# Performance work log

Measured on AMD Instinct MI355X. Metric: run time of the kernel, lower is better.

## Reference

```python
import jax, jax.numpy as jnp
import numpy as np

B, S, H = 32, 1, 1024            # decode: one query token per sequence
NH, HD = 16, 64                  # num_heads, head_dim
BS = 16                          # cache block size
MAX_KV = 2048                    # max sequence length in cache
BLOCKS_PER_SEQ = MAX_KV // BS    # 128
NUM_BLOCKS = B * BLOCKS_PER_SEQ  # 4096 physical blocks
SCALE = HD ** -0.5


def setup_inputs() -> dict:
    key = jax.random.key(0)
    ks = jax.random.split(key, 8)
    hidden_states = jax.random.normal(ks[0], (B, S, H), jnp.float32) * 0.02
    # kv_cache[0] = key cache, kv_cache[1] = value cache; paged layout
    kv_cache = jax.random.normal(ks[1], (2, NUM_BLOCKS, BS, NH, HD), jnp.float32) * 0.02
    # each sequence owns a contiguous run of physical blocks (valid block table)
    block_tables = jnp.arange(NUM_BLOCKS, dtype=jnp.int32).reshape(B, BLOCKS_PER_SEQ)
    seq_lens = jax.random.randint(ks[2], (B,), 1, MAX_KV + 1, dtype=jnp.int32)
    w_attn = jax.random.normal(ks[3], (H, 3 * H), jnp.float32) * 0.02
    b_attn = jax.random.normal(ks[4], (3 * H,), jnp.float32) * 0.02
    w_proj = jax.random.normal(ks[5], (H, H), jnp.float32) * 0.02
    b_proj = jax.random.normal(ks[6], (H,), jnp.float32) * 0.02
    return {"hidden_states": hidden_states, "kv_cache": kv_cache,
            "block_tables": block_tables, "seq_lens": seq_lens,
            "w_attn": w_attn, "b_attn": b_attn,
            "w_proj": w_proj, "b_proj": b_proj}


def reference(hidden_states, kv_cache, block_tables, seq_lens,
              w_attn, b_attn, w_proj, b_proj):
    # qkv projection (c_attn); only q is consumed by the paged-attention decode
    qkv = hidden_states @ w_attn + b_attn                      # [B, S, 3H]
    q = qkv[..., :H].reshape(B, S, NH, HD)                     # [B, 1, NH, HD]

    # block-table gather of paged KV cache
    # kv_cache[0][block_tables]: [B, BLOCKS_PER_SEQ, BS, NH, HD]
    keys = kv_cache[0][block_tables].reshape(B, MAX_KV, NH, HD)
    vals = kv_cache[1][block_tables].reshape(B, MAX_KV, NH, HD)

    scores = jnp.einsum('bsnd,bknd->bnsk', q, keys) * SCALE    # [B, NH, S, MAX_KV]
    valid = jnp.arange(MAX_KV)[None, :] < seq_lens[:, None]    # [B, MAX_KV]
    scores = jnp.where(valid[:, None, None, :], scores, -jnp.inf)
    probs = jax.nn.softmax(scores, axis=-1)

    attn = jnp.einsum('bnsk,bknd->bsnd', probs, vals).reshape(B, S, H)
    return attn @ w_proj + b_proj                              # [B, S, H]
```

## Files before the change

### kernel.cpp

```cpp
#include <hip/hip_runtime.h>
#include <hip/hip_bf16.h>

#define BATCH 32
#define HID 1024
#define NH 16
#define HD 64
#define BS 16
#define MAX_KV 2048
#define BPS 128
#define NUM_BLOCKS 4096
#define SCALE 0.125f

#define SPLITS 8
#define CHUNK 256
#define KSPLIT 4
#define KCHUNK (HID / KSPLIT)

__global__ __launch_bounds__(256) void init_kernel(
    const float* __restrict__ b_attn, const float* __restrict__ b_proj,
    float* __restrict__ q, float* __restrict__ out)
{
    const int i = blockIdx.x * 256 + threadIdx.x;
    const int col = i & (HID - 1);
    q[i]   = b_attn[col];
    out[i] = b_proj[col];
}

__global__ __launch_bounds__(256) void gemv_kernel(
    const float* __restrict__ x,
    const float* __restrict__ w,
    float* __restrict__ y,
    int wstride)
{
    const int colg = blockIdx.x;
    const int kz = blockIdx.y;
    const int tid = threadIdx.x, wave = tid >> 6, lane = tid & 63;
    const int col = colg * 64 + lane;

    __shared__ float s_x[BATCH * KCHUNK];
    for (int i = tid; i < BATCH * KCHUNK; i += 256) {
        const int bb = i >> 8, kk = i & (KCHUNK - 1);
        s_x[bb * KCHUNK + kk] = x[bb * HID + kz * KCHUNK + kk];
    }
    __syncthreads();

    float acc[BATCH];
    #pragma unroll
    for (int b = 0; b < BATCH; ++b) acc[b] = 0.f;

    const int kw = wave * (KCHUNK / 4);
    const float* wp = w + (size_t)(kz * KCHUNK + kw) * wstride + col;
    #pragma unroll 4
    for (int j = 0; j < KCHUNK / 4; ++j) {
        const float wv = wp[(size_t)j * wstride];
        #pragma unroll
        for (int b = 0; b < BATCH; ++b)
            acc[b] += s_x[b * KCHUNK + kw + j] * wv;
    }

    __syncthreads();
    #pragma unroll
    for (int b = 0; b < BATCH; ++b)
        s_x[wave * 2048 + b * 64 + lane] = acc[b];
    __syncthreads();
    for (int i = tid; i < BATCH * 64; i += 256) {
        const int bb = i >> 6, cc = i & 63;
        const float v = s_x[0 * 2048 + bb * 64 + cc] + s_x[1 * 2048 + bb * 64 + cc]
                      + s_x[2 * 2048 + bb * 64 + cc] + s_x[3 * 2048 + bb * 64 + cc];
        atomicAdd(&y[bb * HID + colg * 64 + cc], v);
    }
}

__global__ __launch_bounds__(256) void attn_split_kernel(
    const float* __restrict__ q,
    const float* __restrict__ kv,
    const int* __restrict__ block_tables,
    const int* __restrict__ seq_lens,
    float* __restrict__ part)
{
    const int h = blockIdx.x, b = blockIdx.y, s = blockIdx.z;
    const int tid = threadIdx.x, wave = tid >> 6, lane = tid & 63;
    const int pos_sub = lane >> 4;
    const int d4 = lane & 15;

    float* my_part = part + ((size_t)(b * NH + h) * SPLITS + s) * (HD + 2);
    const int n = seq_lens[b];
    const int p0 = s * CHUNK;

    if (p0 >= n) {
        if (tid < HD) my_part[tid] = 0.f;
        if (tid == 0) { my_part[HD] = -1e30f; my_part[HD + 1] = 0.f; }
        return;
    }
    const int cnt = min(n - p0, CHUNK);

    __shared__ float s_sc[CHUNK];
    __shared__ int   s_bt[CHUNK / BS];
    __shared__ float s_redm[4], s_redl[4];
    __shared__ float s_part[4 * HD];

    if (tid < CHUNK / BS) s_bt[tid] = block_tables[b * BPS + p0 / BS + tid];
    const float4 qv = *reinterpret_cast<const float4*>(
        q + (size_t)(b * NH + h) * HD + d4 * 4);
    __syncthreads();

    const size_t v_off = (size_t)NUM_BLOCKS * BS * NH * HD;

    for (int base = wave * 8; base < cnt; base += 32) {
        const int pa = base + 2 * pos_sub;
        const int pb = pa + 1;
        float sa = 0.f, sb = 0.f;
        if (pa < cnt) {
            const float* kp = kv + (((size_t)s_bt[pa >> 4] * BS + (pa & 15)) * NH + h) * HD + d4 * 4;
            const float4 k4 = *reinterpret_cast<const float4*>(kp);
            sa = qv.x * k4.x + qv.y * k4.y + qv.z * k4.z + qv.w * k4.w;
        }
        if (pb < cnt) {
            const float* kp = kv + (((size_t)s_bt[pb >> 4] * BS + (pb & 15)) * NH + h) * HD + d4 * 4;
            const float4 k4 = *reinterpret_cast<const float4*>(kp);
            sb = qv.x * k4.x + qv.y * k4.y + qv.z * k4.z + qv.w * k4.w;
        }
        sa += __shfl_xor(sa, 1); sb += __shfl_xor(sb, 1);
        sa += __shfl_xor(sa, 2); sb += __shfl_xor(sb, 2);
        sa += __shfl_xor(sa, 4); sb += __shfl_xor(sb, 4);
        sa += __shfl_xor(sa, 8); sb += __shfl_xor(sb, 8);
        if (d4 == 0) {
            if (pa < cnt) s_sc[pa] = sa * SCALE;
            if (pb < cnt) s_sc[pb] = sb * SCALE;
        }
    }
    __syncthreads();

    const float v = (tid < cnt) ? s_sc[tid] : -1e30f;
    float m = v;
    #pragma unroll
    for (int msk = 32; msk; msk >>= 1) m = fmaxf(m, __shfl_xor(m, msk));
    if (lane == 0) s_redm[wave] = m;
    __syncthreads();
    m = fmaxf(fmaxf(s_redm[0], s_redm[1]), fmaxf(s_redm[2], s_redm[3]));

    const float e = (tid < cnt) ? __expf(v - m) : 0.f;
    if (tid < cnt) s_sc[tid] = e;
    float l = e;
    #pragma unroll
    for (int msk = 32; msk; msk >>= 1) l += __shfl_xor(l, msk);
    if (lane == 0) s_redl[wave] = l;
    __syncthreads();
    const float l_tot = s_redl[0] + s_redl[1] + s_redl[2] + s_redl[3];

    float4 acc = {0.f, 0.f, 0.f, 0.f};
    for (int base = wave * 8; base < cnt; base += 32) {
        const int pa = base + 2 * pos_sub;
        const int pb = pa + 1;
        if (pa < cnt) {
            const float* vp = kv + v_off + (((size_t)s_bt[pa >> 4] * BS + (pa & 15)) * NH + h) * HD + d4 * 4;
            const float4 v4 = *reinterpret_cast<const float4*>(vp);
            const float w = s_sc[pa];
            acc.x += w * v4.x; acc.y += w * v4.y; acc.z += w * v4.z; acc.w += w * v4.w;
        }
        if (pb < cnt) {
            const float* vp = kv + v_off + (((size_t)s_bt[pb >> 4] * BS + (pb & 15)) * NH + h) * HD + d4 * 4;
            const float4 v4 = *reinterpret_cast<const float4*>(vp);
            const float w = s_sc[pb];
            acc.x += w * v4.x; acc.y += w * v4.y; acc.z += w * v4.z; acc.w += w * v4.w;
        }
    }
    acc.x += __shfl_xor(acc.x, 16); acc.y += __shfl_xor(acc.y, 16);
    acc.z += __shfl_xor(acc.z, 16); acc.w += __shfl_xor(acc.w, 16);
    acc.x += __shfl_xor(acc.x, 32); acc.y += __shfl_xor(acc.y, 32);
    acc.z += __shfl_xor(acc.z, 32); acc.w += __shfl_xor(acc.w, 32);
    if (pos_sub == 0) {
        s_part[wave * HD + d4 * 4 + 0] = acc.x;
        s_part[wave * HD + d4 * 4 + 1] = acc.y;
        s_part[wave * HD + d4 * 4 + 2] = acc.z;
        s_part[wave * HD + d4 * 4 + 3] = acc.w;
    }
    __syncthreads();
    if (tid < HD) {
        my_part[tid] = s_part[tid] + s_part[HD + tid] +
                       s_part[2 * HD + tid] + s_part[3 * HD + tid];
    }
    if (tid == 0) { my_part[HD] = m; my_part[HD + 1] = l_tot; }
}

__global__ __launch_bounds__(64) void attn_reduce_kernel(
    const float* __restrict__ part,
    float* __restrict__ attn_out)
{
    const int h = blockIdx.x, b = blockIdx.y, d = threadIdx.x;
    const float* pp = part + (size_t)(b * NH + h) * SPLITS * (HD + 2);
    float m = -1e30f;
    #pragma unroll
    for (int s = 0; s < SPLITS; ++s) m = fmaxf(m, pp[s * (HD + 2) + HD]);
    float o = 0.f, l = 0.f;
    #pragma unroll
    for (int s = 0; s < SPLITS; ++s) {
        const float a = __expf(pp[s * (HD + 2) + HD] - m);
        o += a * pp[s * (HD + 2) + d];
        l += a * pp[s * (HD + 2) + HD + 1];
    }
    attn_out[(size_t)b * HID + h * HD + d] = o / l;
}

extern "C" void kernel_launch(void* const* d_in, const int* in_sizes, int n_in,
                              void* d_out, int out_size, void* d_ws, size_t ws_size,
                              hipStream_t stream) {
    const float* hs     = (const float*)d_in[0];
    const float* kv     = (const float*)d_in[1];
    const int*   bt     = (const int*)d_in[2];
    const int*   sl     = (const int*)d_in[3];
    const float* w_attn = (const float*)d_in[4];
    const float* b_attn = (const float*)d_in[5];
    const float* w_proj = (const float*)d_in[6];
    const float* b_proj = (const float*)d_in[7];
    float* out = (float*)d_out;

    float* q    = (float*)d_ws;
    float* attn = q + BATCH * HID;
    float* part = attn + BATCH * HID;

    init_kernel<<<BATCH * HID / 256, 256, 0, stream>>>(b_attn, b_proj, q, out);
    gemv_kernel<<<dim3(HID / 64, KSPLIT), 256, 0, stream>>>(hs, w_attn, q, 3 * HID);
    attn_split_kernel<<<dim3(NH, BATCH, SPLITS), 256, 0, stream>>>(q, kv, bt, sl, part);
    attn_reduce_kernel<<<dim3(NH, BATCH), 64, 0, stream>>>(part, attn);
    gemv_kernel<<<dim3(HID / 64, KSPLIT), 256, 0, stream>>>(attn, w_proj, out, HID);
}
```

Measured before the change: 702.3 us.

## Increase split counts, restructure GEMV per-wave batching, unroll attention loads, skip empty splits

The GEMV now uses 16 K-splits, with each wave owning 8 batch rows across the whole K chunk. It reads float4 activations from shared memory and atomically adds results directly, which drops the cross-wave shared reduction. Attention uses 16 splits of 128 positions and issues 4 loads per lane per iteration for more memory-level parallelism. Scale is folded into q, and empty splits exit early, with the reduce kernel reading only the live splits based on seq_lens. More atomics and more blocks add contention and launch overhead.

```diff
diff --git a/kernel.cpp b/kernel.cpp
--- a/kernel.cpp
+++ b/kernel.cpp
@@ -11,9 +11,9 @@
 #define NUM_BLOCKS 4096
 #define SCALE 0.125f
 
-#define SPLITS 8
-#define CHUNK 256
-#define KSPLIT 4
+#define SPLITS 16
+#define CHUNK 128
+#define KSPLIT 16
 #define KCHUNK (HID / KSPLIT)
 
 __global__ __launch_bounds__(256) void init_kernel(
@@ -37,38 +37,35 @@
     const int tid = threadIdx.x, wave = tid >> 6, lane = tid & 63;
     const int col = colg * 64 + lane;
 
-    __shared__ float s_x[BATCH * KCHUNK];
+    __shared__ __align__(16) float s_x[BATCH * KCHUNK];
     for (int i = tid; i < BATCH * KCHUNK; i += 256) {
-        const int bb = i >> 8, kk = i & (KCHUNK - 1);
-        s_x[bb * KCHUNK + kk] = x[bb * HID + kz * KCHUNK + kk];
-    }
-    __syncthreads();
-
-    float acc[BATCH];
-    #pragma unroll
-    for (int b = 0; b < BATCH; ++b) acc[b] = 0.f;
-
-    const int kw = wave * (KCHUNK / 4);
-    const float* wp = w + (size_t)(kz * KCHUNK + kw) * wstride + col;
-    #pragma unroll 4
-    for (int j = 0; j < KCHUNK / 4; ++j) {
-        const float wv = wp[(size_t)j * wstride];
-        #pragma unroll
-        for (int b = 0; b < BATCH; ++b)
-            acc[b] += s_x[b * KCHUNK + kw + j] * wv;
-    }
-
-    __syncthreads();
-    #pragma unroll
-    for (int b = 0; b < BATCH; ++b)
-        s_x[wave * 2048 + b * 64 + lane] = acc[b];
-    __syncthreads();
-    for (int i = tid; i < BATCH * 64; i += 256) {
-        const int bb = i >> 6, cc = i & 63;
-        const float v = s_x[0 * 2048 + bb * 64 + cc] + s_x[1 * 2048 + bb * 64 + cc]
-                      + s_x[2 * 2048 + bb * 64 + cc] + s_x[3 * 2048 + bb * 64 + cc];
-        atomicAdd(&y[bb * HID + colg * 64 + cc], v);
-    }
+        const int bb = i >> 6, kk = i & (KCHUNK - 1);
+        s_x[i] = x[bb * HID + kz * KCHUNK + kk];
+    }
+    __syncthreads();
+
+    const int b0 = wave * 8;
+    float acc[8];
+    #pragma unroll
+    for (int b = 0; b < 8; ++b) acc[b] = 0.f;
+
+    const float4* s_x4 = reinterpret_cast<const float4*>(s_x);
+    const float* wp = w + (size_t)(kz * KCHUNK) * wstride + col;
+    #pragma unroll
+    for (int jb = 0; jb < KCHUNK / 4; ++jb) {
+        const float wv0 = wp[(size_t)(jb * 4 + 0) * wstride];
+        const float wv1 = wp[(size_t)(jb * 4 + 1) * wstride];
+        const float wv2 = wp[(size_t)(jb * 4 + 2) * wstride];
+        const float wv3 = wp[(size_t)(jb * 4 + 3) * wstride];
+        #pragma unroll
+        for (int b = 0; b < 8; ++b) {
+            const float4 xv = s_x4[(b0 + b) * (KCHUNK / 4) + jb];
+            acc[b] += xv.x * wv0 + xv.y * wv1 + xv.z * wv2 + xv.w * wv3;
+        }
+    }
+    #pragma unroll
+    for (int b = 0; b < 8; ++b)
+        atomicAdd(&y[(size_t)(b0 + b) * HID + col], acc[b]);
 }
 
 __global__ __launch_bounds__(256) void attn_split_kernel(
@@ -79,54 +76,50 @@
     float* __restrict__ part)
 {
     const int h = blockIdx.x, b = blockIdx.y, s = blockIdx.z;
+    const int n = seq_lens[b];
+    const int p0 = s * CHUNK;
+    if (p0 >= n) return;
+    const int cnt = min(n - p0, CHUNK);
+
     const int tid = threadIdx.x, wave = tid >> 6, lane = tid & 63;
     const int pos_sub = lane >> 4;
     const int d4 = lane & 15;
 
     float* my_part = part + ((size_t)(b * NH + h) * SPLITS + s) * (HD + 2);
-    const int n = seq_lens[b];
-    const int p0 = s * CHUNK;
-
-    if (p0 >= n) {
-        if (tid < HD) my_part[tid] = 0.f;
-        if (tid == 0) { my_part[HD] = -1e30f; my_part[HD + 1] = 0.f; }
-        return;
-    }
-    const int cnt = min(n - p0, CHUNK);
 
     __shared__ float s_sc[CHUNK];
     __shared__ int   s_bt[CHUNK / BS];
     __shared__ float s_redm[4], s_redl[4];
     __shared__ float s_part[4 * HD];
 
-    if (tid < CHUNK / BS) s_bt[tid] = block_tables[b * BPS + p0 / BS + tid];
-    const float4 qv = *reinterpret_cast<const float4*>(
+    if (tid < CHUNK / BS) s_bt[tid] = block_tables[b * BPS + s * (CHUNK / BS) + tid];
+    float4 qv = *reinterpret_cast<const float4*>(
         q + (size_t)(b * NH + h) * HD + d4 * 4);
+    qv.x *= SCALE; qv.y *= SCALE; qv.z *= SCALE; qv.w *= SCALE;
     __syncthreads();
 
     const size_t v_off = (size_t)NUM_BLOCKS * BS * NH * HD;
 
-    for (int base = wave * 8; base < cnt; base += 32) {
-        const int pa = base + 2 * pos_sub;
-        const int pb = pa + 1;
-        float sa = 0.f, sb = 0.f;
-        if (pa < cnt) {
-            const float* kp = kv + (((size_t)s_bt[pa >> 4] * BS + (pa & 15)) * NH + h) * HD + d4 * 4;
-            const float4 k4 = *reinterpret_cast<const float4*>(kp);
-            sa = qv.x * k4.x + qv.y * k4.y + qv.z * k4.z + qv.w * k4.w;
-        }
-        if (pb < cnt) {
-            const float* kp = kv + (((size_t)s_bt[pb >> 4] * BS + (pb & 15)) * NH + h) * HD + d4 * 4;
-            const float4 k4 = *reinterpret_cast<const float4*>(kp);
-            sb = qv.x * k4.x + qv.y * k4.y + qv.z * k4.z + qv.w * k4.w;
-        }
-        sa += __shfl_xor(sa, 1); sb += __shfl_xor(sb, 1);
-        sa += __shfl_xor(sa, 2); sb += __shfl_xor(sb, 2);
-        sa += __shfl_xor(sa, 4); sb += __shfl_xor(sb, 4);
-        sa += __shfl_xor(sa, 8); sb += __shfl_xor(sb, 8);
-        if (d4 == 0) {
-            if (pa < cnt) s_sc[pa] = sa * SCALE;
-            if (pb < cnt) s_sc[pb] = sb * SCALE;
+    for (int base = wave * 16; base < cnt; base += 64) {
+        float sc[4];
+        #pragma unroll
+        for (int u = 0; u < 4; ++u) {
+            const int p = base + 4 * pos_sub + u;
+            sc[u] = 0.f;
+            if (p < cnt) {
+                const float* kp = kv + (((size_t)s_bt[p >> 4] * BS + (p & 15)) * NH + h) * HD + d4 * 4;
+                const float4 k4 = *reinterpret_cast<const float4*>(kp);
+                sc[u] = qv.x * k4.x + qv.y * k4.y + qv.z * k4.z + qv.w * k4.w;
+            }
+        }
+        #pragma unroll
+        for (int u = 0; u < 4; ++u) {
+            sc[u] += __shfl_xor(sc[u], 1);
+            sc[u] += __shfl_xor(sc[u], 2);
+            sc[u] += __shfl_xor(sc[u], 4);
+            sc[u] += __shfl_xor(sc[u], 8);
+            const int p = base + 4 * pos_sub + u;
+            if (d4 == 0 && p < cnt) s_sc[p] = sc[u];
         }
     }
     __syncthreads();
@@ -149,20 +142,17 @@
     const float l_tot = s_redl[0] + s_redl[1] + s_redl[2] + s_redl[3];
 
     float4 acc = {0.f, 0.f, 0.f, 0.f};
-    for (int base = wave * 8; base < cnt; base += 32) {
-        const int pa = base + 2 * pos_sub;
-        const int pb = pa + 1;
-        if (pa < cnt) {
-            const float* vp = kv + v_off + (((size_t)s_bt[pa >> 4] * BS + (pa & 15)) * NH + h) * HD + d4 * 4;
-            const float4 v4 = *reinterpret_cast<const float4*>(vp);
-            const float w = s_sc[pa];
-            acc.x += w * v4.x; acc.y += w * v4.y; acc.z += w * v4.z; acc.w += w * v4.w;
-        }
-        if (pb < cnt) {
-            const float* vp = kv + v_off + (((size_t)s_bt[pb >> 4] * BS + (pb & 15)) * NH + h) * HD + d4 * 4;
-            const float4 v4 = *reinterpret_cast<const float4*>(vp);
-            const float w = s_sc[pb];
-            acc.x += w * v4.x; acc.y += w * v4.y; acc.z += w * v4.z; acc.w += w * v4.w;
+    for (int base = wave * 16; base < cnt; base += 64) {
+        #pragma unroll
+        for (int u = 0; u < 4; ++u) {
+            const int p = base + 4 * pos_sub + u;
+            if (p < cnt) {
+                const float* vp = kv + v_off + (((size_t)s_bt[p >> 4] * BS + (p & 15)) * NH + h) * HD + d4 * 4;
+                const float4 v4 = *reinterpret_cast<const float4*>(vp);
+                const float w = s_sc[p];
+                acc.x += w * v4.x; acc.y += w * v4.y;
+                acc.z += w * v4.z; acc.w += w * v4.w;
+            }
         }
     }
     acc.x += __shfl_xor(acc.x, 16); acc.y += __shfl_xor(acc.y, 16);
@@ -185,16 +175,17 @@
 
 __global__ __launch_bounds__(64) void attn_reduce_kernel(
     const float* __restrict__ part,
+    const int* __restrict__ seq_lens,
     float* __restrict__ attn_out)
 {
     const int h = blockIdx.x, b = blockIdx.y, d = threadIdx.x;
+    const int n = seq_lens[b];
+    const int ns = (n + CHUNK - 1) / CHUNK;
     const float* pp = part + (size_t)(b * NH + h) * SPLITS * (HD + 2);
     float m = -1e30f;
-    #pragma unroll
-    for (int s = 0; s < SPLITS; ++s) m = fmaxf(m, pp[s * (HD + 2) + HD]);
+    for (int s = 0; s < ns; ++s) m = fmaxf(m, pp[s * (HD + 2) + HD]);
     float o = 0.f, l = 0.f;
-    #pragma unroll
-    for (int s = 0; s < SPLITS; ++s) {
+    for (int s = 0; s < ns; ++s) {
         const float a = __expf(pp[s * (HD + 2) + HD] - m);
         o += a * pp[s * (HD + 2) + d];
         l += a * pp[s * (HD + 2) + HD + 1];
@@ -222,6 +213,6 @@
     init_kernel<<<BATCH * HID / 256, 256, 0, stream>>>(b_attn, b_proj, q, out);
     gemv_kernel<<<dim3(HID / 64, KSPLIT), 256, 0, stream>>>(hs, w_attn, q, 3 * HID);
     attn_split_kernel<<<dim3(NH, BATCH, SPLITS), 256, 0, stream>>>(q, kv, bt, sl, part);
-    attn_reduce_kernel<<<dim3(NH, BATCH), 64, 0, stream>>>(part, attn);
+    attn_reduce_kernel<<<dim3(NH, BATCH), 64, 0, stream>>>(part, sl, attn);
     gemv_kernel<<<dim3(HID / 64, KSPLIT), 256, 0, stream>>>(attn, w_proj, out, HID);
 }
```

New measurement: 691.5 us. Within noise of the previous version (-1.5%).
